# Performance work log

Measured on AMD Instinct MI355X. Metric: run time of the kernel, lower is better.

## Reference

```python
import jax, jax.numpy as jnp
import numpy as np
import math

SIZE = 64
SCALE = math.sqrt(SIZE)
EPS = 1e-12  # torch F.normalize default eps

def l2_normalize(x, axis):
    n = jnp.linalg.norm(x, ord=2, axis=axis, keepdims=True)
    return x / jnp.maximum(n, EPS)

def setup_inputs() -> dict:
    key = jax.random.key(0)
    k1, k2, k3 = jax.random.split(key, 3)
    n, l, s, d, v = 8, 2048, 2048, SIZE, SIZE
    return {
        "query": jax.random.normal(k1, (n, l, d), dtype=jnp.float32),
        "key": jax.random.normal(k2, (n, s, d), dtype=jnp.float32),
        "value": jax.random.normal(k3, (n, s, v), dtype=jnp.float32),
        "mask": jnp.ones((n, l, s), dtype=bool),
    }

def reference(query, key, value, mask):
    # rank-3 query path with normalize=True (cosine attention)
    q = l2_normalize(query, 2)
    k = l2_normalize(key, 2)
    score = jnp.einsum('nlk,nsk->nls', q, k) / SCALE
    score = jnp.where(mask, score, -jnp.inf)
    score = jax.nn.softmax(score, axis=2)  # [n, l, s]
    # equivalent to (score.unsqueeze(3) * value.unsqueeze(1)).sum(2)
    output_value = jnp.einsum('nls,nsv->nlv', score, value)
    return (output_value, score)
```

## Files before the change

### kernel.cpp

```cpp
#include <hip/hip_runtime.h>
#include <hip/hip_bf16.h>
#include <math.h>


typedef __bf16 bf16x8 __attribute__((ext_vector_type(8)));
typedef __bf16 bf16x4 __attribute__((ext_vector_type(4)));
typedef float f32x4 __attribute__((ext_vector_type(4)));

#define NB 8
#define LL 2048
#define SS 2048
#define DD 64
#define WORDS (SS / 32)

__global__ __launch_bounds__(256) void pack_mask(const int* __restrict__ mask,
                                                 unsigned long long* __restrict__ bm) {
  const int w = threadIdx.x >> 6, lane = threadIdx.x & 63;
  const size_t gw = (size_t)blockIdx.x * 4 + w;
  const size_t stride = (size_t)gridDim.x * 4;
#pragma unroll
  for (int i = 0; i < 4; ++i) {
    size_t seg = gw + (size_t)i * stride;
    int m = __builtin_nontemporal_load(mask + seg * 64 + lane);
    unsigned long long b = __ballot(m != 0);
    if (lane == 0) bm[seg] = b;
  }
}

__global__ __launch_bounds__(256) void prep_norm(const float* __restrict__ q,
                                                 const float* __restrict__ k,
                                                 __bf16* __restrict__ Qb,
                                                 __bf16* __restrict__ Kb) {
  int w = threadIdx.x >> 6, lane = threadIdx.x & 63;
  int r = blockIdx.x * 4 + w;
  const float* src;
  __bf16* dst;
  float extra;
  if (r < NB * LL) {
    src = q + (size_t)r * DD;
    dst = Qb + (size_t)r * DD;
    extra = 0.125f;
  } else {
    int rk = r - NB * LL;
    src = k + (size_t)rk * DD;
    dst = Kb + (size_t)rk * DD;
    extra = 1.0f;
  }
  float x = src[lane];
  float ss = x * x;
  ss += __shfl_xor(ss, 1);
  ss += __shfl_xor(ss, 2);
  ss += __shfl_xor(ss, 4);
  ss += __shfl_xor(ss, 8);
  ss += __shfl_xor(ss, 16);
  ss += __shfl_xor(ss, 32);
  float nrm = sqrtf(ss);
  float sc = extra / fmaxf(nrm, 1e-12f);
  dst[lane] = (__bf16)(x * sc);
}

__global__ __launch_bounds__(256) void prep_vt(const float* __restrict__ v,
                                               __bf16* __restrict__ Vt) {
  __shared__ __bf16 tile[64][72];
  int n = blockIdx.y;
  int s0 = blockIdx.x * 64;
  int t = threadIdx.x;
#pragma unroll
  for (int it = 0; it < 4; ++it) {
    int idx = t + it * 256;
    int s = idx >> 4, c = idx & 15;
    float4 f = *(const float4*)(v + ((size_t)(n * SS + s0 + s)) * DD + c * 4);
    tile[s][c * 4 + 0] = (__bf16)f.x;
    tile[s][c * 4 + 1] = (__bf16)f.y;
    tile[s][c * 4 + 2] = (__bf16)f.z;
    tile[s][c * 4 + 3] = (__bf16)f.w;
  }
  __syncthreads();
#pragma unroll
  for (int it = 0; it < 4; ++it) {
    int idx = t + it * 256;
    int vv = idx >> 4, c = idx & 15;
    bf16x4 o;
    o[0] = tile[c * 4 + 0][vv];
    o[1] = tile[c * 4 + 1][vv];
    o[2] = tile[c * 4 + 2][vv];
    o[3] = tile[c * 4 + 3][vv];
    *(bf16x4*)(Vt + ((size_t)(n * DD + vv)) * SS + s0 + c * 4) = o;
  }
}

__global__ __launch_bounds__(256, 4) void attn_main(const __bf16* __restrict__ Qb,
                                                    const __bf16* __restrict__ Kb,
                                                    const __bf16* __restrict__ Vt,
                                                    const unsigned* __restrict__ bm32,
                                                    float* __restrict__ out_val,
                                                    float* __restrict__ out_score) {
  __shared__ __bf16 e_lds[2][16][72];
  __shared__ float rs_lds[4][16];
  __shared__ unsigned bm_t[WORDS][16];

  const int n = blockIdx.y;
  const int l0 = blockIdx.x * 16;
  const int t = threadIdx.x;
  const int w = t >> 6;
  const int lane = t & 63;
  const int m16 = lane & 15;
  const int quad = lane >> 4;

  {
    int word = t & 63, wv = t >> 6;
#pragma unroll
    for (int i = 0; i < 4; ++i) {
      int row = wv * 4 + i;
      bm_t[word][row] = bm32[(((size_t)(n * LL + l0 + row)) << 6) + word];
    }
  }

  const __bf16* qrow = Qb + ((size_t)(n * LL + l0 + m16)) * DD;
  bf16x8 aq0 = *(const bf16x8*)(qrow + quad * 8);
  bf16x8 aq1 = *(const bf16x8*)(qrow + 32 + quad * 8);

  const __bf16* kbase = Kb + (size_t)n * SS * DD;
  const __bf16* vbase = Vt + (size_t)n * DD * SS + (size_t)(16 * w + m16) * SS;
  const size_t mrow_base = ((size_t)(n * LL + l0)) * SS;
  const int scol_off = w * 16 + m16;
  const unsigned shift = (unsigned)(scol_off & 31);
  const int word_off = scol_off >> 5;

  f32x4 acc_o = {0.f, 0.f, 0.f, 0.f};
  float rsum[4] = {0.f, 0.f, 0.f, 0.f};

  const __bf16* krow0 = kbase + (size_t)scol_off * DD;
  bf16x8 kb0 = *(const bf16x8*)(krow0 + quad * 8);
  bf16x8 kb1 = *(const bf16x8*)(krow0 + 32 + quad * 8);
  bf16x8 vb0 = *(const bf16x8*)(vbase + quad * 8);
  bf16x8 vb1 = *(const bf16x8*)(vbase + 32 + quad * 8);

  __syncthreads();

  for (int c = 0; c < SS / 64; ++c) {
    const int cn = (c + 1) & 31;
    const __bf16* krow_n = kbase + (size_t)(cn * 64 + scol_off) * DD;
    bf16x8 nkb0 = *(const bf16x8*)(krow_n + quad * 8);
    bf16x8 nkb1 = *(const bf16x8*)(krow_n + 32 + quad * 8);
    bf16x8 nvb0 = *(const bf16x8*)(vbase + cn * 64 + quad * 8);
    bf16x8 nvb1 = *(const bf16x8*)(vbase + cn * 64 + 32 + quad * 8);

    f32x4 acc = {0.f, 0.f, 0.f, 0.f};
    acc = __builtin_amdgcn_mfma_f32_16x16x32_bf16(aq0, kb0, acc, 0, 0, 0);
    acc = __builtin_amdgcn_mfma_f32_16x16x32_bf16(aq1, kb1, acc, 0, 0, 0);

    const uint4 mw = *(const uint4*)&bm_t[c * 2 + word_off][quad * 4];
#pragma unroll
    for (int r = 0; r < 4; ++r) {
      unsigned mk = ((&mw.x)[r] >> shift) & 1u;
      float e = mk ? __expf(acc[r]) : 0.0f;
      rsum[r] += e;
      e_lds[c & 1][quad * 4 + r][w * 16 + m16] = (__bf16)e;
    }
    __syncthreads();

    bf16x8 ae0 = *(const bf16x8*)(&e_lds[c & 1][m16][quad * 8]);
    bf16x8 ae1 = *(const bf16x8*)(&e_lds[c & 1][m16][32 + quad * 8]);
    acc_o = __builtin_amdgcn_mfma_f32_16x16x32_bf16(ae0, vb0, acc_o, 0, 0, 0);
    acc_o = __builtin_amdgcn_mfma_f32_16x16x32_bf16(ae1, vb1, acc_o, 0, 0, 0);

    kb0 = nkb0; kb1 = nkb1; vb0 = nvb0; vb1 = nvb1;
  }

#pragma unroll
  for (int r = 0; r < 4; ++r) {
    float s = rsum[r];
    s += __shfl_xor(s, 1);
    s += __shfl_xor(s, 2);
    s += __shfl_xor(s, 4);
    s += __shfl_xor(s, 8);
    rsum[r] = s;
  }
  if (m16 == 0) {
#pragma unroll
    for (int r = 0; r < 4; ++r) rs_lds[w][quad * 4 + r] = rsum[r];
  }
  __syncthreads();
  float inv[4];
#pragma unroll
  for (int r = 0; r < 4; ++r) {
    int row = quad * 4 + r;
    float s = rs_lds[0][row] + rs_lds[1][row] + rs_lds[2][row] + rs_lds[3][row];
    inv[r] = 1.0f / s;
  }

#pragma unroll
  for (int r = 0; r < 4; ++r) {
    int row = quad * 4 + r;
    out_val[((size_t)(n * LL + l0 + row)) * DD + 16 * w + m16] = acc_o[r] * inv[r];
  }

  bf16x8 pk0 = *(const bf16x8*)(krow0 + quad * 8);
  bf16x8 pk1 = *(const bf16x8*)(krow0 + 32 + quad * 8);
  for (int c = 0; c < SS / 64; ++c) {
    const int cn = (c + 1) & 31;
    const __bf16* krow_n = kbase + (size_t)(cn * 64 + scol_off) * DD;
    bf16x8 nk0 = *(const bf16x8*)(krow_n + quad * 8);
    bf16x8 nk1 = *(const bf16x8*)(krow_n + 32 + quad * 8);

    f32x4 acc = {0.f, 0.f, 0.f, 0.f};
    acc = __builtin_amdgcn_mfma_f32_16x16x32_bf16(aq0, pk0, acc, 0, 0, 0);
    acc = __builtin_amdgcn_mfma_f32_16x16x32_bf16(aq1, pk1, acc, 0, 0, 0);

    const uint4 mw = *(const uint4*)&bm_t[c * 2 + word_off][quad * 4];
    const int scol = c * 64 + scol_off;
#pragma unroll
    for (int r = 0; r < 4; ++r) {
      unsigned mk = ((&mw.x)[r] >> shift) & 1u;
      float val = mk ? __expf(acc[r]) * inv[r] : 0.0f;
      size_t idx = mrow_base + (size_t)(quad * 4 + r) * SS + scol;
      __builtin_nontemporal_store(val, out_score + idx);
    }
    pk0 = nk0; pk1 = nk1;
  }
}

extern "C" void kernel_launch(void* const* d_in, const int* in_sizes, int n_in,
                              void* d_out, int out_size, void* d_ws, size_t ws_size,
                              hipStream_t stream) {
  const float* q = (const float*)d_in[0];
  const float* k = (const float*)d_in[1];
  const float* v = (const float*)d_in[2];
  const int* mask = (const int*)d_in[3];

  float* out_val = (float*)d_out;
  float* out_score = out_val + (size_t)NB * LL * DD;

  __bf16* Qb = (__bf16*)d_ws;
  __bf16* Kb = Qb + (size_t)NB * LL * DD;
  __bf16* Vt = Kb + (size_t)NB * SS * DD;
  unsigned long long* bm = (unsigned long long*)(Vt + (size_t)NB * DD * SS);

  pack_mask<<<dim3(32768), dim3(256), 0, stream>>>(mask, bm);
  prep_norm<<<dim3((NB * LL * 2) / 4), dim3(256), 0, stream>>>(q, k, Qb, Kb);
  prep_vt<<<dim3(SS / 64, NB), dim3(256), 0, stream>>>(v, Vt);
  attn_main<<<dim3(LL / 16, NB), dim3(256), 0, stream>>>(Qb, Kb, Vt, (const unsigned*)bm,
                                                         out_val, out_score);
}
```

Before: 339.6 us.

## Split key dimension across waves with per-wave strips, remove per-chunk block barriers

Each of the four waves now owns a 512-column strip of the key sequence and computes the full 64-wide output for its strip, instead of all waves cooperating on each 64-column chunk. Per-chunk __syncthreads are no longer needed because each wave has its own e_lds buffer. Partial outputs are reduced across waves through LDS reused from the same shared allocation. Score stores switch from nontemporal to plain stores, and the register prefetching of K/V for the next chunk is dropped, which raises register pressure and may expose load latency.

```diff
diff --git a/kernel.cpp b/kernel.cpp
--- a/kernel.cpp
+++ b/kernel.cpp
@@ -12,6 +12,7 @@
 #define SS 2048
 #define DD 64
 #define WORDS (SS / 32)
+#define STRIP 512
 
 __global__ __launch_bounds__(256) void pack_mask(const int* __restrict__ mask,
                                                  unsigned long long* __restrict__ bm) {
@@ -95,9 +96,11 @@
                                                     const unsigned* __restrict__ bm32,
                                                     float* __restrict__ out_val,
                                                     float* __restrict__ out_score) {
-  __shared__ __bf16 e_lds[2][16][72];
-  __shared__ float rs_lds[4][16];
-  __shared__ unsigned bm_t[WORDS][16];
+  __shared__ char smem[22784];
+  __bf16(*e_lds)[2][16][72] = (__bf16(*)[2][16][72])smem;
+  unsigned(*bm_t)[16] = (unsigned(*)[16])(smem + 18432);
+  float(*rs_lds)[16] = (float(*)[16])(smem + 22528);
+  float(*o_lds)[16][64] = (float(*)[16][64])smem;
 
   const int n = blockIdx.y;
   const int l0 = blockIdx.x * 16;
@@ -121,51 +124,54 @@
   bf16x8 aq1 = *(const bf16x8*)(qrow + 32 + quad * 8);
 
   const __bf16* kbase = Kb + (size_t)n * SS * DD;
-  const __bf16* vbase = Vt + (size_t)n * DD * SS + (size_t)(16 * w + m16) * SS;
+  const __bf16* vbase = Vt + (size_t)n * DD * SS;
   const size_t mrow_base = ((size_t)(n * LL + l0)) * SS;
-  const int scol_off = w * 16 + m16;
-  const unsigned shift = (unsigned)(scol_off & 31);
-  const int word_off = scol_off >> 5;
-
-  f32x4 acc_o = {0.f, 0.f, 0.f, 0.f};
+  const int sbase = w * STRIP;
+
+  f32x4 acc_o[4] = {{0.f, 0.f, 0.f, 0.f}, {0.f, 0.f, 0.f, 0.f},
+                    {0.f, 0.f, 0.f, 0.f}, {0.f, 0.f, 0.f, 0.f}};
   float rsum[4] = {0.f, 0.f, 0.f, 0.f};
 
-  const __bf16* krow0 = kbase + (size_t)scol_off * DD;
-  bf16x8 kb0 = *(const bf16x8*)(krow0 + quad * 8);
-  bf16x8 kb1 = *(const bf16x8*)(krow0 + 32 + quad * 8);
-  bf16x8 vb0 = *(const bf16x8*)(vbase + quad * 8);
-  bf16x8 vb1 = *(const bf16x8*)(vbase + 32 + quad * 8);
-
-  __syncthreads();
-
-  for (int c = 0; c < SS / 64; ++c) {
-    const int cn = (c + 1) & 31;
-    const __bf16* krow_n = kbase + (size_t)(cn * 64 + scol_off) * DD;
-    bf16x8 nkb0 = *(const bf16x8*)(krow_n + quad * 8);
-    bf16x8 nkb1 = *(const bf16x8*)(krow_n + 32 + quad * 8);
-    bf16x8 nvb0 = *(const bf16x8*)(vbase + cn * 64 + quad * 8);
-    bf16x8 nvb1 = *(const bf16x8*)(vbase + cn * 64 + 32 + quad * 8);
-
-    f32x4 acc = {0.f, 0.f, 0.f, 0.f};
-    acc = __builtin_amdgcn_mfma_f32_16x16x32_bf16(aq0, kb0, acc, 0, 0, 0);
-    acc = __builtin_amdgcn_mfma_f32_16x16x32_bf16(aq1, kb1, acc, 0, 0, 0);
-
-    const uint4 mw = *(const uint4*)&bm_t[c * 2 + word_off][quad * 4];
-#pragma unroll
-    for (int r = 0; r < 4; ++r) {
-      unsigned mk = ((&mw.x)[r] >> shift) & 1u;
-      float e = mk ? __expf(acc[r]) : 0.0f;
-      rsum[r] += e;
-      e_lds[c & 1][quad * 4 + r][w * 16 + m16] = (__bf16)e;
-    }
-    __syncthreads();
-
-    bf16x8 ae0 = *(const bf16x8*)(&e_lds[c & 1][m16][quad * 8]);
-    bf16x8 ae1 = *(const bf16x8*)(&e_lds[c & 1][m16][32 + quad * 8]);
-    acc_o = __builtin_amdgcn_mfma_f32_16x16x32_bf16(ae0, vb0, acc_o, 0, 0, 0);
-    acc_o = __builtin_amdgcn_mfma_f32_16x16x32_bf16(ae1, vb1, acc_o, 0, 0, 0);
-
-    kb0 = nkb0; kb1 = nkb1; vb0 = nvb0; vb1 = nvb1;
+  __syncthreads();
+
+  for (int c = 0; c < STRIP / 64; ++c) {
+    const int s0 = sbase + c * 64;
+    f32x4 acc[4];
+#pragma unroll
+    for (int ct = 0; ct < 4; ++ct) {
+      const __bf16* krow = kbase + (size_t)(s0 + ct * 16 + m16) * DD;
+      bf16x8 kb0 = *(const bf16x8*)(krow + quad * 8);
+      bf16x8 kb1 = *(const bf16x8*)(krow + 32 + quad * 8);
+      f32x4 a = {0.f, 0.f, 0.f, 0.f};
+      a = __builtin_amdgcn_mfma_f32_16x16x32_bf16(aq0, kb0, a, 0, 0, 0);
+      a = __builtin_amdgcn_mfma_f32_16x16x32_bf16(aq1, kb1, a, 0, 0, 0);
+      acc[ct] = a;
+    }
+    const int bw = s0 >> 5;
+    const uint4 mw0 = *(const uint4*)&bm_t[bw][quad * 4];
+    const uint4 mw1 = *(const uint4*)&bm_t[bw + 1][quad * 4];
+#pragma unroll
+    for (int ct = 0; ct < 4; ++ct) {
+      const unsigned sh = (unsigned)((ct * 16 + m16) & 31);
+#pragma unroll
+      for (int r = 0; r < 4; ++r) {
+        unsigned wd = (ct < 2) ? (&mw0.x)[r] : (&mw1.x)[r];
+        unsigned mk = (wd >> sh) & 1u;
+        float e = mk ? __expf(acc[ct][r]) : 0.0f;
+        rsum[r] += e;
+        e_lds[w][c & 1][quad * 4 + r][ct * 16 + m16] = (__bf16)e;
+      }
+    }
+    bf16x8 ae0 = *(const bf16x8*)(&e_lds[w][c & 1][m16][quad * 8]);
+    bf16x8 ae1 = *(const bf16x8*)(&e_lds[w][c & 1][m16][32 + quad * 8]);
+#pragma unroll
+    for (int vt = 0; vt < 4; ++vt) {
+      const __bf16* vrow = vbase + (size_t)(vt * 16 + m16) * SS + s0;
+      bf16x8 vb0 = *(const bf16x8*)(vrow + quad * 8);
+      bf16x8 vb1 = *(const bf16x8*)(vrow + 32 + quad * 8);
+      acc_o[vt] = __builtin_amdgcn_mfma_f32_16x16x32_bf16(ae0, vb0, acc_o[vt], 0, 0, 0);
+      acc_o[vt] = __builtin_amdgcn_mfma_f32_16x16x32_bf16(ae1, vb1, acc_o[vt], 0, 0, 0);
+    }
   }
 
 #pragma unroll
@@ -177,11 +183,19 @@
     s += __shfl_xor(s, 8);
     rsum[r] = s;
   }
+
+  __syncthreads();
+
+#pragma unroll
+  for (int vt = 0; vt < 4; ++vt)
+#pragma unroll
+    for (int r = 0; r < 4; ++r) o_lds[w][quad * 4 + r][vt * 16 + m16] = acc_o[vt][r];
   if (m16 == 0) {
 #pragma unroll
     for (int r = 0; r < 4; ++r) rs_lds[w][quad * 4 + r] = rsum[r];
   }
   __syncthreads();
+
   float inv[4];
 #pragma unroll
   for (int r = 0; r < 4; ++r) {
@@ -189,35 +203,41 @@
     float s = rs_lds[0][row] + rs_lds[1][row] + rs_lds[2][row] + rs_lds[3][row];
     inv[r] = 1.0f / s;
   }
-
 #pragma unroll
   for (int r = 0; r < 4; ++r) {
     int row = quad * 4 + r;
-    out_val[((size_t)(n * LL + l0 + row)) * DD + 16 * w + m16] = acc_o[r] * inv[r];
-  }
-
-  bf16x8 pk0 = *(const bf16x8*)(krow0 + quad * 8);
-  bf16x8 pk1 = *(const bf16x8*)(krow0 + 32 + quad * 8);
-  for (int c = 0; c < SS / 64; ++c) {
-    const int cn = (c + 1) & 31;
-    const __bf16* krow_n = kbase + (size_t)(cn * 64 + scol_off) * DD;
-    bf16x8 nk0 = *(const bf16x8*)(krow_n + quad * 8);
-    bf16x8 nk1 = *(const bf16x8*)(krow_n + 32 + quad * 8);
-
-    f32x4 acc = {0.f, 0.f, 0.f, 0.f};
-    acc = __builtin_amdgcn_mfma_f32_16x16x32_bf16(aq0, pk0, acc, 0, 0, 0);
-    acc = __builtin_amdgcn_mfma_f32_16x16x32_bf16(aq1, pk1, acc, 0, 0, 0);
-
-    const uint4 mw = *(const uint4*)&bm_t[c * 2 + word_off][quad * 4];
-    const int scol = c * 64 + scol_off;
-#pragma unroll
-    for (int r = 0; r < 4; ++r) {
-      unsigned mk = ((&mw.x)[r] >> shift) & 1u;
-      float val = mk ? __expf(acc[r]) * inv[r] : 0.0f;
-      size_t idx = mrow_base + (size_t)(quad * 4 + r) * SS + scol;
-      __builtin_nontemporal_store(val, out_score + idx);
-    }
-    pk0 = nk0; pk1 = nk1;
+    float o = o_lds[0][row][16 * w + m16] + o_lds[1][row][16 * w + m16] +
+              o_lds[2][row][16 * w + m16] + o_lds[3][row][16 * w + m16];
+    out_val[((size_t)(n * LL + l0 + row)) * DD + 16 * w + m16] = o * inv[r];
+  }
+
+  for (int c = 0; c < STRIP / 64; ++c) {
+    const int s0 = sbase + c * 64;
+    f32x4 acc[4];
+#pragma unroll
+    for (int ct = 0; ct < 4; ++ct) {
+      const __bf16* krow = kbase + (size_t)(s0 + ct * 16 + m16) * DD;
+      bf16x8 kb0 = *(const bf16x8*)(krow + quad * 8);
+      bf16x8 kb1 = *(const bf16x8*)(krow + 32 + quad * 8);
+      f32x4 a = {0.f, 0.f, 0.f, 0.f};
+      a = __builtin_amdgcn_mfma_f32_16x16x32_bf16(aq0, kb0, a, 0, 0, 0);
+      a = __builtin_amdgcn_mfma_f32_16x16x32_bf16(aq1, kb1, a, 0, 0, 0);
+      acc[ct] = a;
+    }
+    const int bw = s0 >> 5;
+    const uint4 mw0 = *(const uint4*)&bm_t[bw][quad * 4];
+    const uint4 mw1 = *(const uint4*)&bm_t[bw + 1][quad * 4];
+#pragma unroll
+    for (int ct = 0; ct < 4; ++ct) {
+      const unsigned sh = (unsigned)((ct * 16 + m16) & 31);
+#pragma unroll
+      for (int r = 0; r < 4; ++r) {
+        unsigned wd = (ct < 2) ? (&mw0.x)[r] : (&mw1.x)[r];
+        unsigned mk = (wd >> sh) & 1u;
+        float val = mk ? __expf(acc[ct][r]) * inv[r] : 0.0f;
+        out_score[mrow_base + (size_t)(quad * 4 + r) * SS + s0 + ct * 16 + m16] = val;
+      }
+    }
   }
 }
 
```

Result: no change. 340.7 us (+0.3%).
